# Kernel tuning notes

Hardware: AMD Instinct MI355X
Metric: run time of the kernel (lower is better)

The kernel has to match this reference:

```python
import jax, jax.numpy as jnp
import numpy as np

N_NODES = 50000
N_EDGES = 800000
N_GRAPHS = 128
IN_CH, HIDDEN, OUT_CH = 16, 64, 2


def gcn_conv(x, src, dst, W, b, n_nodes):
    """GCNConv: add self-loops, sym-normalized adjacency scatter-add, linear."""
    h = x @ W  # [N, H]
    loop = jnp.arange(n_nodes, dtype=src.dtype)
    s = jnp.concatenate([src, loop])  # [E+N]
    d = jnp.concatenate([dst, loop])
    deg = jax.ops.segment_sum(jnp.ones_like(d, dtype=h.dtype), d, num_segments=n_nodes)
    dinv = jnp.where(deg > 0, jax.lax.rsqrt(deg), 0.0)  # deg^{-1/2}
    norm = dinv[s] * dinv[d]  # [E+N]
    msg = h[s] * norm[:, None]  # gather + scale, [E+N, H]
    out = jax.ops.segment_sum(msg, d, num_segments=n_nodes)  # scatter-add
    return out + b


def global_mean_pool(x, batch, n_graphs):
    sums = jax.ops.segment_sum(x, batch, num_segments=n_graphs)
    cnts = jax.ops.segment_sum(jnp.ones((x.shape[0],), x.dtype), batch, num_segments=n_graphs)
    return sums / jnp.maximum(cnts, 1.0)[:, None]


def setup_inputs() -> dict:
    key = jax.random.key(0)
    ks = jax.random.split(key, 10)
    x = jax.random.normal(ks[0], (N_NODES, IN_CH), dtype=jnp.float32)
    edge_index = jax.random.randint(ks[1], (2, N_EDGES), 0, N_NODES, dtype=jnp.int64)
    batch = jnp.sort(jax.random.randint(ks[2], (N_NODES,), 0, N_GRAPHS, dtype=jnp.int64))
    def glorot(k, shp):
        lim = float(np.sqrt(6.0 / (shp[0] + shp[1])))
        return jax.random.uniform(k, shp, jnp.float32, -lim, lim)
    W1 = glorot(ks[3], (IN_CH, HIDDEN))
    b1 = jnp.zeros((HIDDEN,), jnp.float32)
    W2 = glorot(ks[4], (HIDDEN, HIDDEN))
    b2 = jnp.zeros((HIDDEN,), jnp.float32)
    Wc = glorot(ks[5], (HIDDEN, OUT_CH))
    bc = jnp.zeros((OUT_CH,), jnp.float32)
    return {"x": x, "edge_index": edge_index, "batch": batch,
            "W1": W1, "b1": b1, "W2": W2, "b2": b2, "Wc": Wc, "bc": bc}


def reference(x, edge_index, batch, W1, b1, W2, b2, Wc, bc):
    src, dst = edge_index[0], edge_index[1]
    n = x.shape[0]
    h = jax.nn.relu(gcn_conv(x, src, dst, W1, b1, n))
    # dropout p=0.3 is identity in eval mode
    h = jax.nn.relu(gcn_conv(h, src, dst, W2, b2, n))
    g = global_mean_pool(h, batch, N_GRAPHS)  # [G, H]
    return g @ Wc + bc  # [G, out_channels]
```

## Files before the change

### kernel.cpp

```cpp
#include <hip/hip_runtime.h>
#include <hip/hip_bf16.h>

#define N_NODES 50000
#define N_EDGES 800000
#define N_GRAPHS 128
#define IN_CH 16
#define HIDDEN 64
#define OUT_CH 2

#define BSHIFT 7
#define BNODES 128
#define NB ((N_NODES + BNODES - 1) / BNODES)
#define BCAP 3072
#define ECHUNK 4096
#define EB ((N_EDGES + ECHUNK - 1) / ECHUNK)
#define MAXK 12
#define EPT 16
#define WT1_LD 18
#define AGG_LD 72
#define W2T_ENT (HIDDEN * AGG_LD)

typedef __attribute__((ext_vector_type(8))) short bf16x8;
typedef __attribute__((ext_vector_type(4))) float f32x4;

__device__ __forceinline__ float bf2f(unsigned short u) {
    return __uint_as_float(((unsigned)u) << 16);
}
__device__ __forceinline__ unsigned short f2bf(float f) {
    __hip_bfloat16 h = __float2bfloat16(f);
    return *reinterpret_cast<unsigned short*>(&h);
}


__global__ void bucket_scatter_kernel(const int* __restrict__ src, const int* __restrict__ dst,
                                      int* __restrict__ bh, int* __restrict__ bh2,
                                      int* __restrict__ pairs,
                                      const float* __restrict__ W2, unsigned short* __restrict__ w2t) {
    __shared__ int lh[NB];
    __shared__ int lstart[NB];
    __shared__ int spair[256];
    int t = threadIdx.x;
    if (blockIdx.x == 0) {
        for (int i = t; i < HIDDEN * HIDDEN; i += 256) {
            int k = i >> 6, c = i & 63;
            w2t[c * AGG_LD + k] = f2bf(W2[i]);
        }
    }
    for (int i = t; i < NB; i += 256) lh[i] = 0;
    __syncthreads();

    int base = blockIdx.x * ECHUNK;
    int nE = N_EDGES - base;
    if (nE > ECHUNK) nE = ECHUNK;

    int ed[EPT], es[EPT];
#pragma unroll
    for (int k = 0; k < EPT; k++) {
        int i = k * 256 + t;
        if (i < nE) {
            ed[k] = dst[base + i];
            es[k] = src[base + i];
        } else {
            ed[k] = -1;
            es[k] = 0;
        }
    }
#pragma unroll
    for (int k = 0; k < EPT; k++)
        if ((unsigned)ed[k] < N_NODES) atomicAdd(&lh[ed[k] >> BSHIFT], 1);
    __syncthreads();

    int a0 = (2 * t < NB) ? lh[2 * t] : 0;
    int a1 = (2 * t + 1 < NB) ? lh[2 * t + 1] : 0;
    spair[t] = a0 + a1;
    __syncthreads();
    for (int off = 1; off < 256; off <<= 1) {
        int u = (t >= off) ? spair[t - off] : 0;
        __syncthreads();
        spair[t] += u;
        __syncthreads();
    }
    int ex = spair[t] - (a0 + a1);
    if (2 * t < NB) lstart[2 * t] = ex;
    if (2 * t + 1 < NB) lstart[2 * t + 1] = ex + a0;
    __syncthreads();

    for (int i = t; i < NB; i += 256) {
        bh[i * EB + blockIdx.x] = lh[i];
        bh2[i * EB + blockIdx.x] = base + lstart[i];
        lh[i] = 0;
    }
    __syncthreads();

#pragma unroll
    for (int k = 0; k < EPT; k++) {
        if ((unsigned)ed[k] < N_NODES) {
            int b = ed[k] >> BSHIFT;
            int r = atomicAdd(&lh[b], 1);
            pairs[base + lstart[b] + r] = (es[k] << BSHIFT) | (ed[k] & (BNODES - 1));
        }
    }
}


__global__ void bucket_csr_kernel(const int* __restrict__ pairs, const int* __restrict__ bh,
                                  const int* __restrict__ bh2,
                                  int* __restrict__ csr, int* __restrict__ rowptr,
                                  int* __restrict__ cnt_node, float* __restrict__ dinv,
                                  const float* __restrict__ x, unsigned short* __restrict__ xs,
                                  float* __restrict__ sums, float* __restrict__ cntg) {
    __shared__ int segaddr[EB];
    __shared__ int pref[EB];
    __shared__ int ptmp[256];
    __shared__ int lcnt[BNODES];
    __shared__ int lsc[BNODES];
    __shared__ int lrow[BNODES];
    __shared__ float sdv[BNODES];
    int b = blockIdx.x;
    int t = threadIdx.x;

    if (b == 0) {
        for (int i = t; i < N_GRAPHS * HIDDEN; i += 256) sums[i] = 0.0f;
        if (t < N_GRAPHS) cntg[t] = 0.0f;
    }

    int cntv = (t < EB) ? bh[b * EB + t] : 0;
    if (t < EB) segaddr[t] = bh2[b * EB + t];
    if (t < BNODES) lcnt[t] = 0;
    ptmp[t] = cntv;
    __syncthreads();
    for (int off = 1; off < 256; off <<= 1) {
        int u = (t >= off) ? ptmp[t - off] : 0;
        __syncthreads();
        ptmp[t] += u;
        __syncthreads();
    }
    if (t < EB) pref[t] = ptmp[t];
    __syncthreads();
    int K = pref[EB - 1];
    if (K > BCAP) K = BCAP;

    int myp[MAXK], myr[MAXK];
#pragma unroll
    for (int k = 0; k < MAXK; k++) {
        int i = k * 256 + t;
        myp[k] = -1;
        if (i < K) {
            int lo = 0, hi = EB - 1;
            while (lo < hi) {
                int mid = (lo + hi) >> 1;
                if (pref[mid] > i) hi = mid; else lo = mid + 1;
            }
            int excl = (lo > 0) ? pref[lo - 1] : 0;
            int p = pairs[segaddr[lo] + (i - excl)];
            myp[k] = p;
            myr[k] = atomicAdd(&lcnt[p & (BNODES - 1)], 1);
        }
    }
    __syncthreads();
    if (t < BNODES) lsc[t] = lcnt[t];
    __syncthreads();
    for (int off = 1; off < BNODES; off <<= 1) {
        int u = (t >= off && t < BNODES) ? lsc[t - off] : 0;
        __syncthreads();
        if (t < BNODES) lsc[t] += u;
        __syncthreads();
    }
    int bstart = b * BCAP;
    if (t < BNODES) {
        int ex = lsc[t] - lcnt[t];
        lrow[t] = ex;
        float dv = rsqrtf((float)(lcnt[t] + 1));
        sdv[t] = dv;
        int n = b * BNODES + t;
        if (n < N_NODES) {
            rowptr[n] = bstart + ex;
            cnt_node[n] = lcnt[t];
            dinv[n] = dv;
        }
    }
    __syncthreads();
#pragma unroll
    for (int k = 0; k < MAXK; k++) {
        if (myp[k] >= 0)
            csr[bstart + lrow[myp[k] & (BNODES - 1)] + myr[k]] = myp[k] >> BSHIFT;
    }
    for (int i = t; i < BNODES * IN_CH; i += 256) {
        int nl = i >> 4;
        int n = b * BNODES + nl;
        if (n < N_NODES) xs[n * IN_CH + (i & 15)] = f2bf(sdv[nl] * x[n * IN_CH + (i & 15)]);
    }
}


__global__ void fused_l1_kernel(const unsigned short* __restrict__ xs, const int* __restrict__ csr_src,
                                const int* __restrict__ rowptr, const int* __restrict__ cnt,
                                const float* __restrict__ dinv, const float* __restrict__ W,
                                const float* __restrict__ b, __hip_bfloat16* __restrict__ h) {
    __shared__ float sWT[HIDDEN * WT1_LD];
    __shared__ float sx[16 * IN_CH];
    int t = threadIdx.x;
    for (int i = t; i < IN_CH * HIDDEN; i += 256) {
        int k = i >> 6, c = i & 63;
        sWT[c * WT1_LD + k] = W[i];
    }

    int n0 = blockIdx.x * 16;
    int w = t >> 6;
    int lane = t & 63;
    int e16 = lane >> 2;
    int cc = (lane & 3) * 4;

    int lens[4], starts[4];
#pragma unroll
    for (int q = 0; q < 4; q++) {
        int n = n0 + w * 4 + q;
        lens[q] = cnt[n];
        starts[q] = rowptr[n];
    }

    for (int q = 0; q < 4; q++) {
        int row = w * 4 + q;
        int n = n0 + row;
        int len = lens[q];
        int start = starts[q];
        int last = len - 1;
        int iters = (len + 31) >> 5;
        float4 acc = make_float4(0.f, 0.f, 0.f, 0.f);
        for (int m = 0; m < iters; m++) {
            int base = m * 32 + e16;
#pragma unroll
            for (int k = 0; k < 2; k++) {
                int j = base + 16 * k;
                int jj = j <= last ? j : last;
                float msk = j <= last ? 1.0f : 0.0f;
                int s = csr_src[start + jj];
                ushort4 xv = *(const ushort4*)&xs[s * IN_CH + cc];
                acc.x += msk * bf2f(xv.x);
                acc.y += msk * bf2f(xv.y);
                acc.z += msk * bf2f(xv.z);
                acc.w += msk * bf2f(xv.w);
            }
        }
#pragma unroll
        for (int m = 4; m <= 32; m <<= 1) {
            acc.x += __shfl_xor(acc.x, m, 64);
            acc.y += __shfl_xor(acc.y, m, 64);
            acc.z += __shfl_xor(acc.z, m, 64);
            acc.w += __shfl_xor(acc.w, m, 64);
        }
        if (lane < 4) {
            float dn = dinv[n];
            ushort4 xsv = *(const ushort4*)&xs[n * IN_CH + cc];
            float4 v;
            v.x = dn * (acc.x + bf2f(xsv.x));
            v.y = dn * (acc.y + bf2f(xsv.y));
            v.z = dn * (acc.z + bf2f(xsv.z));
            v.w = dn * (acc.w + bf2f(xsv.w));
            *(float4*)&sx[row * IN_CH + cc] = v;
        }
    }
    __syncthreads();

    int r = w;
    int c = t & 63;
    float bias = b[c];
#pragma unroll
    for (int nb = 0; nb < 4; nb++) {
        int row = nb * 4 + r;
        int n = n0 + row;
        if (n >= N_NODES) continue;
        float acch = bias;
#pragma unroll
        for (int k4 = 0; k4 < IN_CH; k4 += 4) {
            float4 a = *(const float4*)&sx[row * IN_CH + k4];
            float2 w0 = *(const float2*)&sWT[c * WT1_LD + k4];
            float2 w1 = *(const float2*)&sWT[c * WT1_LD + k4 + 2];
            acch += a.x * w0.x + a.y * w0.y + a.z * w1.x + a.w * w1.y;
        }
        float v = acch > 0.0f ? acch : 0.0f;
        h[n * HIDDEN + c] = __float2bfloat16(dinv[n] * v);
    }
}


__global__ void fused_l2_kernel(const __hip_bfloat16* __restrict__ h, const int* __restrict__ csr_src,
                                const int* __restrict__ rowptr, const int* __restrict__ cnt,
                                const float* __restrict__ dinv, const unsigned short* __restrict__ w2t,
                                const float* __restrict__ b, const int* __restrict__ batch,
                                float* __restrict__ sums, float* __restrict__ cntg) {
    __shared__ unsigned short sW[W2T_ENT];
    __shared__ unsigned short sagg[16 * AGG_LD];
    int t = threadIdx.x;
    {
        const uint4* wp = (const uint4*)w2t;
        uint4* sWv = (uint4*)sW;
#pragma unroll
        for (int i = 0; i < 3; i++) {
            int idx = i * 256 + t;
            if (idx < W2T_ENT / 8) sWv[idx] = wp[idx];
        }
    }

    int n0 = blockIdx.x * 16;
    int w = t >> 6;
    int lane = t & 63;
    int e8 = lane >> 3;
    int cc8 = (lane & 7) * 8;
    const unsigned short* hu = (const unsigned short*)h;

    int lens[4], starts[4];
#pragma unroll
    for (int q = 0; q < 4; q++) {
        int n = n0 + w * 4 + q;
        lens[q] = cnt[n];
        starts[q] = rowptr[n];
    }

    for (int q = 0; q < 4; q++) {
        int row = w * 4 + q;
        int n = n0 + row;
        int len = lens[q];
        int start = starts[q];
        int last = len - 1;
        int iters = (len + 31) >> 5;
        float4 alo = make_float4(0.f, 0.f, 0.f, 0.f);
        float4 ahi = make_float4(0.f, 0.f, 0.f, 0.f);
        for (int m = 0; m < iters; m++) {
            int base = m * 32 + e8;
#pragma unroll
            for (int k = 0; k < 4; k++) {
                int j = base + 8 * k;
                int jj = j <= last ? j : last;
                float msk = j <= last ? 1.0f : 0.0f;
                int s = csr_src[start + jj];
                uint4 raw = *(const uint4*)&hu[s * HIDDEN + cc8];
                alo.x += msk * __uint_as_float(raw.x << 16);
                alo.y += msk * __uint_as_float(raw.x & 0xffff0000u);
                alo.z += msk * __uint_as_float(raw.y << 16);
                alo.w += msk * __uint_as_float(raw.y & 0xffff0000u);
                ahi.x += msk * __uint_as_float(raw.z << 16);
                ahi.y += msk * __uint_as_float(raw.z & 0xffff0000u);
                ahi.z += msk * __uint_as_float(raw.w << 16);
                ahi.w += msk * __uint_as_float(raw.w & 0xffff0000u);
            }
        }
#pragma unroll
        for (int m = 8; m <= 32; m <<= 1) {
            alo.x += __shfl_xor(alo.x, m, 64);
            alo.y += __shfl_xor(alo.y, m, 64);
            alo.z += __shfl_xor(alo.z, m, 64);
            alo.w += __shfl_xor(alo.w, m, 64);
            ahi.x += __shfl_xor(ahi.x, m, 64);
            ahi.y += __shfl_xor(ahi.y, m, 64);
            ahi.z += __shfl_xor(ahi.z, m, 64);
            ahi.w += __shfl_xor(ahi.w, m, 64);
        }
        if (lane < 8) {
            uint4 sv = *(const uint4*)&hu[n * HIDDEN + cc8];
            float dn = dinv[n];
            ushort4 o0, o1;
            o0.x = f2bf(dn * (alo.x + __uint_as_float(sv.x << 16)));
            o0.y = f2bf(dn * (alo.y + __uint_as_float(sv.x & 0xffff0000u)));
            o0.z = f2bf(dn * (alo.z + __uint_as_float(sv.y << 16)));
            o0.w = f2bf(dn * (alo.w + __uint_as_float(sv.y & 0xffff0000u)));
            o1.x = f2bf(dn * (ahi.x + __uint_as_float(sv.z << 16)));
            o1.y = f2bf(dn * (ahi.y + __uint_as_float(sv.z & 0xffff0000u)));
            o1.z = f2bf(dn * (ahi.z + __uint_as_float(sv.w << 16)));
            o1.w = f2bf(dn * (ahi.w + __uint_as_float(sv.w & 0xffff0000u)));
            *(ushort4*)&sagg[row * AGG_LD + cc8] = o0;
            *(ushort4*)&sagg[row * AGG_LD + cc8 + 4] = o1;
        }
    }
    __syncthreads();

    int quad = lane >> 4;
    int col = lane & 15;
    int cch = w * 16 + col;
    bf16x8 a0 = *(const bf16x8*)&sagg[col * AGG_LD + quad * 8];
    bf16x8 a1 = *(const bf16x8*)&sagg[col * AGG_LD + 32 + quad * 8];
    bf16x8 b0 = *(const bf16x8*)&sW[cch * AGG_LD + quad * 8];
    bf16x8 b1 = *(const bf16x8*)&sW[cch * AGG_LD + 32 + quad * 8];
    f32x4 d = {0.f, 0.f, 0.f, 0.f};
    d = __builtin_amdgcn_mfma_f32_16x16x32_bf16(a0, b0, d, 0, 0, 0);
    d = __builtin_amdgcn_mfma_f32_16x16x32_bf16(a1, b1, d, 0, 0, 0);
    float bias = b[cch];
    float v[4];
#pragma unroll
    for (int r = 0; r < 4; r++) {
        float z = d[r] + bias;
        v[r] = z > 0.0f ? z : 0.0f;
    }

    int glo = batch[n0];
    int ghi = batch[n0 + 15];
    if (glo == ghi) {
        float s4 = (v[0] + v[1]) + (v[2] + v[3]);
        s4 += __shfl_xor(s4, 16, 64);
        s4 += __shfl_xor(s4, 32, 64);
        if (quad == 0) atomicAdd(&sums[glo * HIDDEN + cch], s4);
        if (t == 0) atomicAdd(&cntg[glo], 16.0f);
    } else {
#pragma unroll
        for (int r = 0; r < 4; r++) {
            int g = batch[n0 + quad * 4 + r];
            if ((unsigned)g < N_GRAPHS) atomicAdd(&sums[g * HIDDEN + cch], v[r]);
        }
        if (w == 0 && col == 0) {
#pragma unroll
            for (int r = 0; r < 4; r++) {
                int g = batch[n0 + quad * 4 + r];
                if ((unsigned)g < N_GRAPHS) atomicAdd(&cntg[g], 1.0f);
            }
        }
    }
}


__global__ void head_kernel(const float* __restrict__ sums, const float* __restrict__ cntg,
                            const float* __restrict__ Wc, const float* __restrict__ bc,
                            float* __restrict__ out) {
    int t = blockIdx.x * blockDim.x + threadIdx.x;
    if (t >= N_GRAPHS * OUT_CH) return;
    int g = t >> 1;
    int o = t & 1;
    float inv = 1.0f / fmaxf(cntg[g], 1.0f);
    float acc = bc[o];
#pragma unroll
    for (int k = 0; k < HIDDEN; k++) acc += sums[g * HIDDEN + k] * inv * Wc[k * OUT_CH + o];
    out[t] = acc;
}


extern "C" void kernel_launch(void* const* d_in, const int* in_sizes, int n_in,
                              void* d_out, int out_size, void* d_ws, size_t ws_size,
                              hipStream_t stream) {
    const float* x  = (const float*)d_in[0];
    const int* ei   = (const int*)d_in[1];
    const int* bat  = (const int*)d_in[2];
    const float* W1 = (const float*)d_in[3];
    const float* b1 = (const float*)d_in[4];
    const float* W2 = (const float*)d_in[5];
    const float* b2 = (const float*)d_in[6];
    const float* Wc = (const float*)d_in[7];
    const float* bc = (const float*)d_in[8];
    float* out = (float*)d_out;

    const int* src = ei;
    const int* dst = ei + N_EDGES;

    char* ws = (char*)d_ws;
    size_t off = 0;
    auto carve = [&](size_t nbytes) {
        char* p = ws + off;
        off += (nbytes + 255) & ~(size_t)255;
        return p;
    };
    float* sums     = (float*)carve(N_GRAPHS * HIDDEN * sizeof(float));
    float* cntg     = (float*)carve(N_GRAPHS * sizeof(float));
    unsigned short* w2t = (unsigned short*)carve(W2T_ENT * sizeof(unsigned short));
    int*   bh       = (int*)carve((size_t)NB * EB * sizeof(int));
    int*   bh2      = (int*)carve((size_t)NB * EB * sizeof(int));
    int*   pairs    = (int*)carve((size_t)EB * ECHUNK * sizeof(int));
    int*   csr      = (int*)carve((size_t)NB * BCAP * sizeof(int));
    int*   rowptr   = (int*)carve(N_NODES * sizeof(int));
    int*   cnt_node = (int*)carve(N_NODES * sizeof(int));
    float* dinv     = (float*)carve(N_NODES * sizeof(float));
    unsigned short* xs = (unsigned short*)carve((size_t)N_NODES * IN_CH * sizeof(unsigned short));
    __hip_bfloat16* bufA = (__hip_bfloat16*)carve((size_t)N_NODES * HIDDEN * sizeof(__hip_bfloat16));
    (void)ws_size;

    const int node16Blk = (N_NODES + 15) / 16;

    bucket_scatter_kernel<<<EB, 256, 0, stream>>>(src, dst, bh, bh2, pairs, W2, w2t);
    bucket_csr_kernel<<<NB, 256, 0, stream>>>(pairs, bh, bh2, csr, rowptr, cnt_node, dinv,
                                              x, xs, sums, cntg);
    fused_l1_kernel<<<node16Blk, 256, 0, stream>>>(xs, csr, rowptr, cnt_node, dinv, W1, b1, bufA);
    fused_l2_kernel<<<node16Blk, 256, 0, stream>>>(bufA, csr, rowptr, cnt_node, dinv, w2t, b2,
                                                   bat, sums, cntg);
    head_kernel<<<1, 256, 0, stream>>>(sums, cntg, Wc, bc, out);
}
```

Baseline: 165.6 us.

## Remap gather lanes to channels, drop shuffle reductions in GCN aggregation kernels

```diff
diff --git a/kernel.cpp b/kernel.cpp
--- a/kernel.cpp
+++ b/kernel.cpp
@@ -208,78 +208,52 @@
     int n0 = blockIdx.x * 16;
     int w = t >> 6;
     int lane = t & 63;
-    int e16 = lane >> 2;
-    int cc = (lane & 3) * 4;
-
-    int lens[4], starts[4];
-#pragma unroll
-    for (int q = 0; q < 4; q++) {
-        int n = n0 + w * 4 + q;
-        lens[q] = cnt[n];
-        starts[q] = rowptr[n];
-    }
-
-    for (int q = 0; q < 4; q++) {
-        int row = w * 4 + q;
-        int n = n0 + row;
-        int len = lens[q];
-        int start = starts[q];
-        int last = len - 1;
-        int iters = (len + 31) >> 5;
-        float4 acc = make_float4(0.f, 0.f, 0.f, 0.f);
-        for (int m = 0; m < iters; m++) {
-            int base = m * 32 + e16;
-#pragma unroll
-            for (int k = 0; k < 2; k++) {
-                int j = base + 16 * k;
-                int jj = j <= last ? j : last;
-                float msk = j <= last ? 1.0f : 0.0f;
-                int s = csr_src[start + jj];
-                ushort4 xv = *(const ushort4*)&xs[s * IN_CH + cc];
-                acc.x += msk * bf2f(xv.x);
-                acc.y += msk * bf2f(xv.y);
-                acc.z += msk * bf2f(xv.z);
-                acc.w += msk * bf2f(xv.w);
-            }
-        }
-#pragma unroll
-        for (int m = 4; m <= 32; m <<= 1) {
-            acc.x += __shfl_xor(acc.x, m, 64);
-            acc.y += __shfl_xor(acc.y, m, 64);
-            acc.z += __shfl_xor(acc.z, m, 64);
-            acc.w += __shfl_xor(acc.w, m, 64);
-        }
-        if (lane < 4) {
-            float dn = dinv[n];
-            ushort4 xsv = *(const ushort4*)&xs[n * IN_CH + cc];
-            float4 v;
-            v.x = dn * (acc.x + bf2f(xsv.x));
-            v.y = dn * (acc.y + bf2f(xsv.y));
-            v.z = dn * (acc.z + bf2f(xsv.z));
-            v.w = dn * (acc.w + bf2f(xsv.w));
-            *(float4*)&sx[row * IN_CH + cc] = v;
-        }
-    }
+    int g = lane >> 4;
+    int c = lane & 15;
+
+    int n_g = n0 + w * 4 + g;
+    int mylen = cnt[n_g];
+    int mystart = rowptr[n_g];
+    int last = mylen - 1;
+    int sguard = (mylen > 0) ? -1 : 0;
+
+    int m1 = mylen;
+    {
+        int o = __shfl_xor(m1, 16, 64); m1 = m1 > o ? m1 : o;
+        o = __shfl_xor(m1, 32, 64);     m1 = m1 > o ? m1 : o;
+    }
+    int lmax = m1;
+
+    float acc = 0.0f;
+    for (int j = 0; j < lmax; ++j) {
+        int jj = j <= last ? j : last;
+        if (jj < 0) jj = 0;
+        float msk = j <= last ? 1.0f : 0.0f;
+        int s = csr_src[mystart + jj] & sguard;
+        acc += msk * bf2f(xs[s * IN_CH + c]);
+    }
+    float dn = dinv[n_g];
+    float v = dn * (acc + bf2f(xs[n_g * IN_CH + c]));
+    sx[(w * 4 + g) * IN_CH + c] = v;
     __syncthreads();
 
     int r = w;
-    int c = t & 63;
-    float bias = b[c];
+    int cB = t & 63;
+    float bias = b[cB];
 #pragma unroll
     for (int nb = 0; nb < 4; nb++) {
         int row = nb * 4 + r;
         int n = n0 + row;
-        if (n >= N_NODES) continue;
         float acch = bias;
 #pragma unroll
         for (int k4 = 0; k4 < IN_CH; k4 += 4) {
             float4 a = *(const float4*)&sx[row * IN_CH + k4];
-            float2 w0 = *(const float2*)&sWT[c * WT1_LD + k4];
-            float2 w1 = *(const float2*)&sWT[c * WT1_LD + k4 + 2];
+            float2 w0 = *(const float2*)&sWT[cB * WT1_LD + k4];
+            float2 w1 = *(const float2*)&sWT[cB * WT1_LD + k4 + 2];
             acch += a.x * w0.x + a.y * w0.y + a.z * w1.x + a.w * w1.y;
         }
-        float v = acch > 0.0f ? acch : 0.0f;
-        h[n * HIDDEN + c] = __float2bfloat16(dinv[n] * v);
+        float vv = acch > 0.0f ? acch : 0.0f;
+        h[n * HIDDEN + cB] = __float2bfloat16(dinv[n] * vv);
     }
 }
 
@@ -305,8 +279,6 @@
     int n0 = blockIdx.x * 16;
     int w = t >> 6;
     int lane = t & 63;
-    int e8 = lane >> 3;
-    int cc8 = (lane & 7) * 8;
     const unsigned short* hu = (const unsigned short*)h;
 
     int lens[4], starts[4];
@@ -317,60 +289,40 @@
         starts[q] = rowptr[n];
     }
 
+#pragma unroll
     for (int q = 0; q < 4; q++) {
         int row = w * 4 + q;
         int n = n0 + row;
         int len = lens[q];
         int start = starts[q];
-        int last = len - 1;
-        int iters = (len + 31) >> 5;
-        float4 alo = make_float4(0.f, 0.f, 0.f, 0.f);
-        float4 ahi = make_float4(0.f, 0.f, 0.f, 0.f);
-        for (int m = 0; m < iters; m++) {
-            int base = m * 32 + e8;
-#pragma unroll
-            for (int k = 0; k < 4; k++) {
-                int j = base + 8 * k;
-                int jj = j <= last ? j : last;
-                float msk = j <= last ? 1.0f : 0.0f;
-                int s = csr_src[start + jj];
-                uint4 raw = *(const uint4*)&hu[s * HIDDEN + cc8];
-                alo.x += msk * __uint_as_float(raw.x << 16);
-                alo.y += msk * __uint_as_float(raw.x & 0xffff0000u);
-                alo.z += msk * __uint_as_float(raw.y << 16);
-                alo.w += msk * __uint_as_float(raw.y & 0xffff0000u);
-                ahi.x += msk * __uint_as_float(raw.z << 16);
-                ahi.y += msk * __uint_as_float(raw.z & 0xffff0000u);
-                ahi.z += msk * __uint_as_float(raw.w << 16);
-                ahi.w += msk * __uint_as_float(raw.w & 0xffff0000u);
+        float a0 = 0.f, a1 = 0.f, a2 = 0.f, a3 = 0.f;
+        if (len > 0) {
+            int last = len - 1;
+            int pl = lane < len ? lane : last;
+            int sidx = csr_src[start + pl];
+            int lim = len < 64 ? len : 64;
+            int j = 0;
+            for (; j + 4 <= lim; j += 4) {
+                int s0 = __builtin_amdgcn_readlane(sidx, j);
+                int s1 = __builtin_amdgcn_readlane(sidx, j + 1);
+                int s2 = __builtin_amdgcn_readlane(sidx, j + 2);
+                int s3 = __builtin_amdgcn_readlane(sidx, j + 3);
+                a0 += bf2f(hu[s0 * HIDDEN + lane]);
+                a1 += bf2f(hu[s1 * HIDDEN + lane]);
+                a2 += bf2f(hu[s2 * HIDDEN + lane]);
+                a3 += bf2f(hu[s3 * HIDDEN + lane]);
             }
-        }
-#pragma unroll
-        for (int m = 8; m <= 32; m <<= 1) {
-            alo.x += __shfl_xor(alo.x, m, 64);
-            alo.y += __shfl_xor(alo.y, m, 64);
-            alo.z += __shfl_xor(alo.z, m, 64);
-            alo.w += __shfl_xor(alo.w, m, 64);
-            ahi.x += __shfl_xor(ahi.x, m, 64);
-            ahi.y += __shfl_xor(ahi.y, m, 64);
-            ahi.z += __shfl_xor(ahi.z, m, 64);
-            ahi.w += __shfl_xor(ahi.w, m, 64);
-        }
-        if (lane < 8) {
-            uint4 sv = *(const uint4*)&hu[n * HIDDEN + cc8];
-            float dn = dinv[n];
-            ushort4 o0, o1;
-            o0.x = f2bf(dn * (alo.x + __uint_as_float(sv.x << 16)));
-            o0.y = f2bf(dn * (alo.y + __uint_as_float(sv.x & 0xffff0000u)));
-            o0.z = f2bf(dn * (alo.z + __uint_as_float(sv.y << 16)));
-            o0.w = f2bf(dn * (alo.w + __uint_as_float(sv.y & 0xffff0000u)));
-            o1.x = f2bf(dn * (ahi.x + __uint_as_float(sv.z << 16)));
-            o1.y = f2bf(dn * (ahi.y + __uint_as_float(sv.z & 0xffff0000u)));
-            o1.z = f2bf(dn * (ahi.z + __uint_as_float(sv.w << 16)));
-            o1.w = f2bf(dn * (ahi.w + __uint_as_float(sv.w & 0xffff0000u)));
-            *(ushort4*)&sagg[row * AGG_LD + cc8] = o0;
-            *(ushort4*)&sagg[row * AGG_LD + cc8 + 4] = o1;
-        }
+            for (; j < lim; ++j) {
+                int s = __builtin_amdgcn_readlane(sidx, j);
+                a0 += bf2f(hu[s * HIDDEN + lane]);
+            }
+            for (; j < len; ++j) {
+                int s = csr_src[start + j];
+                a0 += bf2f(hu[s * HIDDEN + lane]);
+            }
+        }
+        float acc = (a0 + a1) + (a2 + a3) + bf2f(hu[n * HIDDEN + lane]);
+        sagg[row * AGG_LD + lane] = f2bf(dinv[n] * acc);
     }
     __syncthreads();
 
```

New measurement: 181.9 us. 1.1x slower.
